# Optimization experiments

Hardware: AMD Instinct MI355X
Metric: run time of the kernel (lower is better)

The kernel has to match this reference:

```python
import jax, jax.numpy as jnp
import numpy as np
from math import sqrt


def setup_inputs() -> dict:
    key = jax.random.key(0)
    k1, k2, k3 = jax.random.split(key, 3)
    B, L, H, E = 2, 2048, 16, 64
    queries = jax.random.normal(k1, (B, L, H, E), dtype=jnp.float32)
    keys = jax.random.normal(k2, (B, L, H, E), dtype=jnp.float32)
    values = jax.random.normal(k3, (B, L, H, E), dtype=jnp.float32)
    return {"queries": queries, "keys": keys, "values": values}


def reference(queries, keys, values):
    # queries: [B,L,H,E], keys: [B,S,H,E], values: [B,S,H,D]
    B, L, H, E = queries.shape
    S = keys.shape[1]
    scale = 1.0 / sqrt(E)
    # raw scores [B,H,L,S]
    scores = jnp.einsum('blhe,bshe->bhls', queries, keys)
    # triangular causal mask (True above diagonal -> masked)
    causal = jnp.triu(jnp.ones((L, S), dtype=bool), k=1)  # [L,S]
    scores = jnp.where(causal[None, None, :, :], -jnp.inf, scores)
    A = jax.nn.softmax(scale * scores, axis=-1)  # dropout p=0 -> identity
    V = jnp.einsum('bhls,bshd->blhd', A, values)
    return V
```

## Files before the change

### kernel.cpp

```cpp
#include <hip/hip_runtime.h>

typedef __attribute__((ext_vector_type(2))) __fp16 fp16x2;
typedef __attribute__((ext_vector_type(4))) _Float16 half4;
typedef __attribute__((ext_vector_type(8))) _Float16 half8;
typedef __attribute__((ext_vector_type(4))) float floatx4;

typedef union { half8 h8; half4 h4[2]; } h8split;

#define B_SZ  2
#define L_SEQ 2048
#define NH    16
#define EDIM  64
#define LOG2E 1.4426950408889634f
#define QSCALE (0.125f * LOG2E)

__device__ __forceinline__ int swz(int s, int ch) {
    return ch ^ (((s & 7) + 2 * (s >> 4)) & 7);
}

__global__ __launch_bounds__(256, 1)
void convert_kv(const float* __restrict__ K, const float* __restrict__ V,
                _Float16* __restrict__ Kh, _Float16* __restrict__ Vt)
{
    __shared__ __align__(16) _Float16 Tile[64 * 64];
    const int st = blockIdx.x & 31;
    const int h  = (blockIdx.x >> 5) & 15;
    const int b  = blockIdx.x >> 9;
    const int s0 = st * 64;
    const int t  = threadIdx.x;
    const int r  = t >> 2, c = t & 3;
    const size_t bh   = (size_t)b * NH + h;
    const size_t src  = (((size_t)b * L_SEQ + s0 + r) * NH + h) * EDIM + c * 16;
    const size_t cbase = bh * (size_t)(L_SEQ * EDIM) + (size_t)st * 4096;

    {
        const float4* kp = (const float4*)(K + src);
        float4 f[4];
#pragma unroll
        for (int i = 0; i < 4; ++i) f[i] = kp[i];
        _Float16 tmp[16];
#pragma unroll
        for (int i = 0; i < 4; ++i) {
            fp16x2 a  = __builtin_amdgcn_cvt_pkrtz(f[i].x, f[i].y);
            fp16x2 b2 = __builtin_amdgcn_cvt_pkrtz(f[i].z, f[i].w);
            tmp[4*i+0] = (_Float16)a[0];  tmp[4*i+1] = (_Float16)a[1];
            tmp[4*i+2] = (_Float16)b2[0]; tmp[4*i+3] = (_Float16)b2[1];
        }
        _Float16* kd = Kh + cbase + (size_t)(r >> 4) * 1024 + (c >> 1) * 512 + (r & 15) * 8;
        *(half8*)(kd + (((2 * c)     & 3) * 128)) = *(half8*)&tmp[0];
        *(half8*)(kd + (((2 * c + 1) & 3) * 128)) = *(half8*)&tmp[8];
    }
    {
        const float4* vp = (const float4*)(V + src);
        float4 f[4];
#pragma unroll
        for (int i = 0; i < 4; ++i) f[i] = vp[i];
        _Float16 tmp[16];
#pragma unroll
        for (int i = 0; i < 4; ++i) {
            fp16x2 a  = __builtin_amdgcn_cvt_pkrtz(f[i].x, f[i].y);
            fp16x2 b2 = __builtin_amdgcn_cvt_pkrtz(f[i].z, f[i].w);
            tmp[4*i+0] = (_Float16)a[0];  tmp[4*i+1] = (_Float16)a[1];
            tmp[4*i+2] = (_Float16)b2[0]; tmp[4*i+3] = (_Float16)b2[1];
        }
        _Float16* base = &Tile[r * 64];
        *(half8*)(base + swz(r, 2 * c)     * 8) = *(half8*)&tmp[0];
        *(half8*)(base + swz(r, 2 * c + 1) * 8) = *(half8*)&tmp[8];
    }
    __syncthreads();
    {
        const int d = t >> 2, seg = t & 3;
        _Float16 tmp[16];
#pragma unroll
        for (int i = 0; i < 16; ++i) {
            const int s = seg * 16 + i;
            tmp[i] = Tile[s * 64 + swz(s, d >> 3) * 8 + (d & 7)];
        }
        _Float16* vd = Vt + cbase + (size_t)seg * 1024 + (d & 15) * 16 + (d >> 4) * 4;
#pragma unroll
        for (int kg = 0; kg < 4; ++kg)
            *(half4*)(vd + kg * 256) = *(half4*)&tmp[kg * 4];
    }
}

__global__ __launch_bounds__(256, 3)
void fa_fwd(const float* __restrict__ Q, const _Float16* __restrict__ Kh,
            const _Float16* __restrict__ Vt, float* __restrict__ O)
{
    __shared__ float slabL[4][4][17];
    __shared__ __align__(16) float slabO[4][16][68];

    const int i    = blockIdx.x;
    const int bh   = i & 31;
    const int tile = 31 - (i >> 5);
    const int b    = bh >> 4;
    const int h    = bh & 15;
    const int w    = threadIdx.x >> 6;
    const int lane = threadIdx.x & 63;
    const int ln16 = lane & 15;
    const int quad = lane >> 4;
    const int qrow0 = tile * 64;

    half8 qfA[4], qfB[4];
#pragma unroll
    for (int g = 0; g < 4; ++g) {
        const float4* qp = (const float4*)(Q + (((size_t)b * L_SEQ + qrow0 + g * 16 + ln16) * NH + h) * EDIM + quad * 8);
        float4 f0 = qp[0], f1 = qp[1];
        float4 f2 = qp[8], f3 = qp[9];
        fp16x2 t0 = __builtin_amdgcn_cvt_pkrtz(f0.x * QSCALE, f0.y * QSCALE);
        fp16x2 t1 = __builtin_amdgcn_cvt_pkrtz(f0.z * QSCALE, f0.w * QSCALE);
        fp16x2 t2 = __builtin_amdgcn_cvt_pkrtz(f1.x * QSCALE, f1.y * QSCALE);
        fp16x2 t3 = __builtin_amdgcn_cvt_pkrtz(f1.z * QSCALE, f1.w * QSCALE);
        qfA[g][0] = (_Float16)t0[0]; qfA[g][1] = (_Float16)t0[1];
        qfA[g][2] = (_Float16)t1[0]; qfA[g][3] = (_Float16)t1[1];
        qfA[g][4] = (_Float16)t2[0]; qfA[g][5] = (_Float16)t2[1];
        qfA[g][6] = (_Float16)t3[0]; qfA[g][7] = (_Float16)t3[1];
        t0 = __builtin_amdgcn_cvt_pkrtz(f2.x * QSCALE, f2.y * QSCALE);
        t1 = __builtin_amdgcn_cvt_pkrtz(f2.z * QSCALE, f2.w * QSCALE);
        t2 = __builtin_amdgcn_cvt_pkrtz(f3.x * QSCALE, f3.y * QSCALE);
        t3 = __builtin_amdgcn_cvt_pkrtz(f3.z * QSCALE, f3.w * QSCALE);
        qfB[g][0] = (_Float16)t0[0]; qfB[g][1] = (_Float16)t0[1];
        qfB[g][2] = (_Float16)t1[0]; qfB[g][3] = (_Float16)t1[1];
        qfB[g][4] = (_Float16)t2[0]; qfB[g][5] = (_Float16)t2[1];
        qfB[g][6] = (_Float16)t3[0]; qfB[g][7] = (_Float16)t3[1];
    }

    floatx4 acc[4][4];
#pragma unroll
    for (int dt = 0; dt < 4; ++dt)
#pragma unroll
        for (int g = 0; g < 4; ++g) acc[dt][g] = (floatx4){0.f,0.f,0.f,0.f};
    float lp[4] = {0.f, 0.f, 0.f, 0.f};

    const _Float16* kb = Kh + (size_t)bh * (L_SEQ * EDIM) + w * 1024 + lane * 8;
    const _Float16* vb = Vt + (size_t)bh * (L_SEQ * EDIM) + w * 1024 + lane * 16;
    const int nch = tile + 1;

    half8 k0c = *(const half8*)kb;
    half8 k1c = *(const half8*)(kb + 512);
    half8 v01c = *(const half8*)vb;
    half8 v23c = *(const half8*)(vb + 8);

    for (int it = 0; it < nch; ++it) {
        floatx4 st4[4];
#pragma unroll
        for (int g = 0; g < 4; ++g) {
            floatx4 z = (floatx4){0.f,0.f,0.f,0.f};
            z = __builtin_amdgcn_mfma_f32_16x16x32_f16(k0c, qfA[g], z, 0, 0, 0);
            st4[g] = __builtin_amdgcn_mfma_f32_16x16x32_f16(k1c, qfB[g], z, 0, 0, 0);
        }
        if (it + 1 < nch) {
            const _Float16* kp = kb + (size_t)(it + 1) * 4096;
            k0c = *(const half8*)kp;
            k1c = *(const half8*)(kp + 512);
        }

        const bool masked = (it == nch - 1);
        half4 pf[4];
#pragma unroll
        for (int g = 0; g < 4; ++g) {
            float p[4];
#pragma unroll
            for (int r = 0; r < 4; ++r) {
                float e = __builtin_amdgcn_exp2f(st4[g][r]);
                if (masked) {
                    const int key = it * 64 + w * 16 + quad * 4 + r;
                    e = (key <= qrow0 + g * 16 + ln16) ? e : 0.0f;
                }
                p[r] = e;
            }
            lp[g] += (p[0] + p[1]) + (p[2] + p[3]);
            fp16x2 lo = __builtin_amdgcn_cvt_pkrtz(p[0], p[1]);
            fp16x2 hi = __builtin_amdgcn_cvt_pkrtz(p[2], p[3]);
            pf[g][0] = (_Float16)lo[0]; pf[g][1] = (_Float16)lo[1];
            pf[g][2] = (_Float16)hi[0]; pf[g][3] = (_Float16)hi[1];
        }

        h8split u01, u23;
        u01.h8 = v01c;
        u23.h8 = v23c;
        const half4 vc0 = u01.h4[0];
        const half4 vc1 = u01.h4[1];
        const half4 vc2 = u23.h4[0];
        const half4 vc3 = u23.h4[1];
#pragma unroll
        for (int g = 0; g < 4; ++g)
            acc[0][g] = __builtin_amdgcn_mfma_f32_16x16x16f16(vc0, pf[g], acc[0][g], 0, 0, 0);
#pragma unroll
        for (int g = 0; g < 4; ++g)
            acc[1][g] = __builtin_amdgcn_mfma_f32_16x16x16f16(vc1, pf[g], acc[1][g], 0, 0, 0);
#pragma unroll
        for (int g = 0; g < 4; ++g)
            acc[2][g] = __builtin_amdgcn_mfma_f32_16x16x16f16(vc2, pf[g], acc[2][g], 0, 0, 0);
#pragma unroll
        for (int g = 0; g < 4; ++g)
            acc[3][g] = __builtin_amdgcn_mfma_f32_16x16x16f16(vc3, pf[g], acc[3][g], 0, 0, 0);

        if (it + 1 < nch) {
            const _Float16* vp = vb + (size_t)(it + 1) * 4096;
            v01c = *(const half8*)vp;
            v23c = *(const half8*)(vp + 8);
        }
    }

#pragma unroll
    for (int g = 0; g < 4; ++g) {
        lp[g] += __shfl_xor(lp[g], 16);
        lp[g] += __shfl_xor(lp[g], 32);
    }
    if (quad == 0) {
#pragma unroll
        for (int g = 0; g < 4; ++g) slabL[w][g][ln16] = lp[g];
    }

    const int q   = threadIdx.x >> 2;
    const int seg = threadIdx.x & 3;
    float inv = 0.f;
#pragma unroll
    for (int dt = 0; dt < 4; ++dt) {
#pragma unroll
        for (int g = 0; g < 4; ++g)
#pragma unroll
            for (int r = 0; r < 4; ++r)
                slabO[w][quad * 4 + r][g * 16 + ln16] = acc[dt][g][r];
        __syncthreads();
        if (dt == 0) {
            float lt = slabL[0][q >> 4][q & 15] + slabL[1][q >> 4][q & 15]
                     + slabL[2][q >> 4][q & 15] + slabL[3][q >> 4][q & 15];
            inv = 1.0f / lt;
        }
        float o0 = 0.f, o1 = 0.f, o2 = 0.f, o3 = 0.f;
#pragma unroll
        for (int ww = 0; ww < 4; ++ww) {
            o0 += slabO[ww][seg * 4 + 0][q];
            o1 += slabO[ww][seg * 4 + 1][q];
            o2 += slabO[ww][seg * 4 + 2][q];
            o3 += slabO[ww][seg * 4 + 3][q];
        }
        float4 ov = {o0 * inv, o1 * inv, o2 * inv, o3 * inv};
        *(float4*)(O + (((size_t)b * L_SEQ + qrow0 + q) * NH + h) * EDIM + dt * 16 + seg * 4) = ov;
        if (dt < 3) __syncthreads();
    }
}

extern "C" void kernel_launch(void* const* d_in, const int* in_sizes, int n_in,
                              void* d_out, int out_size, void* d_ws, size_t ws_size,
                              hipStream_t stream) {
    const float* Q = (const float*)d_in[0];
    const float* K = (const float*)d_in[1];
    const float* V = (const float*)d_in[2];
    float* O = (float*)d_out;
    _Float16* Kh = (_Float16*)d_ws;
    _Float16* Vt = Kh + (size_t)B_SZ * NH * L_SEQ * EDIM;
    convert_kv<<<dim3(B_SZ * NH * (L_SEQ / 64)), dim3(256), 0, stream>>>(K, V, Kh, Vt);
    fa_fwd<<<dim3(B_SZ * NH * 32), dim3(256), 0, stream>>>(Q, Kh, Vt, O);
}
```

Baseline: 124.5 us.

## Split long causal tiles across two blocks and combine partial results

Query tiles 16-31, which have the longest causal key ranges, are each split into two halves over the key chunks and run as separate blocks, in an interleaved order meant to balance load. Each half writes its unnormalized partial output and row sums to workspace, and a new combine kernel adds the halves and normalizes. This targets tail imbalance in the triangular workload and raises the block count from 1024 to 1536. The cost is an extra kernel launch and extra global traffic for the partials. There is no max-subtraction in the softmax, so the partials can simply be added.

Result: slower. 129.0 us (+3.6%).

```diff
diff --git a/kernel.cpp b/kernel.cpp
--- a/kernel.cpp
+++ b/kernel.cpp
@@ -13,6 +13,8 @@
 #define EDIM  64
 #define LOG2E 1.4426950408889634f
 #define QSCALE (0.125f * LOG2E)
+
+#define PREC 4160
 
 __device__ __forceinline__ int swz(int s, int ch) {
     return ch ^ (((s & 7) + 2 * (s >> 4)) & 7);
@@ -85,14 +87,31 @@
 
 __global__ __launch_bounds__(256, 3)
 void fa_fwd(const float* __restrict__ Q, const _Float16* __restrict__ Kh,
-            const _Float16* __restrict__ Vt, float* __restrict__ O)
+            const _Float16* __restrict__ Vt, float* __restrict__ O,
+            float* __restrict__ P)
 {
     __shared__ float slabL[4][4][17];
     __shared__ __align__(16) float slabO[4][16][68];
 
-    const int i    = blockIdx.x;
-    const int bh   = i & 31;
-    const int tile = 31 - (i >> 5);
+    const int row  = blockIdx.x >> 5;
+    const int bh   = blockIdx.x & 31;
+
+    int tile, half = 0, split = 0;
+    if (row < 4) {
+        if (row == 3) { tile = 15; }
+        else { split = 1; tile = (row == 2) ? 30 : 31; half = (row == 1); }
+    } else if (row < 39) {
+        const int g = (row - 4) / 5, pos = (row - 4) % 5, s = 15 - g;
+        if (pos == 4) { tile = s - 1; }
+        else { split = 1; tile = 2 * s - ((pos + 1) >> 1); half = (pos == 0 || pos == 2); }
+    } else if (row == 39) { split = 1; tile = 16; half = 1; }
+    else { tile = 47 - row; }
+
+    const int mid = (tile + 2) >> 1;
+    const int c0  = (split && half) ? mid : 0;
+    const int c1  = (split && !half) ? mid : tile + 1;
+    const int pidx = split ? (((bh << 4) | (tile - 16)) * 2 + half) : 0;
+
     const int b    = bh >> 4;
     const int h    = bh & 15;
     const int w    = threadIdx.x >> 6;
@@ -134,14 +153,13 @@
 
     const _Float16* kb = Kh + (size_t)bh * (L_SEQ * EDIM) + w * 1024 + lane * 8;
     const _Float16* vb = Vt + (size_t)bh * (L_SEQ * EDIM) + w * 1024 + lane * 16;
-    const int nch = tile + 1;
-
-    half8 k0c = *(const half8*)kb;
-    half8 k1c = *(const half8*)(kb + 512);
-    half8 v01c = *(const half8*)vb;
-    half8 v23c = *(const half8*)(vb + 8);
-
-    for (int it = 0; it < nch; ++it) {
+
+    half8 k0c = *(const half8*)(kb + (size_t)c0 * 4096);
+    half8 k1c = *(const half8*)(kb + (size_t)c0 * 4096 + 512);
+    half8 v01c = *(const half8*)(vb + (size_t)c0 * 4096);
+    half8 v23c = *(const half8*)(vb + (size_t)c0 * 4096 + 8);
+
+    for (int it = c0; it < c1; ++it) {
         floatx4 st4[4];
 #pragma unroll
         for (int g = 0; g < 4; ++g) {
@@ -149,13 +167,13 @@
             z = __builtin_amdgcn_mfma_f32_16x16x32_f16(k0c, qfA[g], z, 0, 0, 0);
             st4[g] = __builtin_amdgcn_mfma_f32_16x16x32_f16(k1c, qfB[g], z, 0, 0, 0);
         }
-        if (it + 1 < nch) {
+        if (it + 1 < c1) {
             const _Float16* kp = kb + (size_t)(it + 1) * 4096;
             k0c = *(const half8*)kp;
             k1c = *(const half8*)(kp + 512);
         }
 
-        const bool masked = (it == nch - 1);
+        const bool masked = (it == tile);
         half4 pf[4];
 #pragma unroll
         for (int g = 0; g < 4; ++g) {
@@ -196,7 +214,7 @@
         for (int g = 0; g < 4; ++g)
             acc[3][g] = __builtin_amdgcn_mfma_f32_16x16x16f16(vc3, pf[g], acc[3][g], 0, 0, 0);
 
-        if (it + 1 < nch) {
+        if (it + 1 < c1) {
             const _Float16* vp = vb + (size_t)(it + 1) * 4096;
             v01c = *(const half8*)vp;
             v23c = *(const half8*)(vp + 8);
@@ -227,7 +245,12 @@
         if (dt == 0) {
             float lt = slabL[0][q >> 4][q & 15] + slabL[1][q >> 4][q & 15]
                      + slabL[2][q >> 4][q & 15] + slabL[3][q >> 4][q & 15];
-            inv = 1.0f / lt;
+            if (split) {
+                if (seg == 0) P[(size_t)pidx * PREC + 4096 + q] = lt;
+                inv = 1.0f;
+            } else {
+                inv = 1.0f / lt;
+            }
         }
         float o0 = 0.f, o1 = 0.f, o2 = 0.f, o3 = 0.f;
 #pragma unroll
@@ -238,8 +261,37 @@
             o3 += slabO[ww][seg * 4 + 3][q];
         }
         float4 ov = {o0 * inv, o1 * inv, o2 * inv, o3 * inv};
-        *(float4*)(O + (((size_t)b * L_SEQ + qrow0 + q) * NH + h) * EDIM + dt * 16 + seg * 4) = ov;
+        const int d = dt * 16 + seg * 4;
+        if (split)
+            *(float4*)(P + (size_t)pidx * PREC + q * 64 + d) = ov;
+        else
+            *(float4*)(O + (((size_t)b * L_SEQ + qrow0 + q) * NH + h) * EDIM + d) = ov;
         if (dt < 3) __syncthreads();
+    }
+}
+
+__global__ __launch_bounds__(256, 1)
+void combine(const float* __restrict__ P, float* __restrict__ O)
+{
+    const int cb  = blockIdx.x;
+    const int bh  = cb & 31;
+    const int tt  = cb >> 5;
+    const int tile = 16 + tt;
+    const int b = bh >> 4, h = bh & 15;
+    const int q   = threadIdx.x >> 2;
+    const int seg = threadIdx.x & 3;
+    const float* A0 = P + (size_t)(((bh << 4) | tt) * 2) * PREC;
+    const float* A1 = A0 + PREC;
+    const float inv = 1.0f / (A0[4096 + q] + A1[4096 + q]);
+    float* op = O + (((size_t)b * L_SEQ + tile * 64 + q) * NH + h) * EDIM;
+#pragma unroll
+    for (int dt = 0; dt < 4; ++dt) {
+        const int d = dt * 16 + seg * 4;
+        float4 a = *(const float4*)(A0 + q * 64 + d);
+        float4 c = *(const float4*)(A1 + q * 64 + d);
+        float4 ov = {(a.x + c.x) * inv, (a.y + c.y) * inv,
+                     (a.z + c.z) * inv, (a.w + c.w) * inv};
+        *(float4*)(op + d) = ov;
     }
 }
 
@@ -252,6 +304,8 @@
     float* O = (float*)d_out;
     _Float16* Kh = (_Float16*)d_ws;
     _Float16* Vt = Kh + (size_t)B_SZ * NH * L_SEQ * EDIM;
+    float* P = (float*)(Vt + (size_t)B_SZ * NH * L_SEQ * EDIM);
     convert_kv<<<dim3(B_SZ * NH * (L_SEQ / 64)), dim3(256), 0, stream>>>(K, V, Kh, Vt);
-    fa_fwd<<<dim3(B_SZ * NH * 32), dim3(256), 0, stream>>>(Q, Kh, Vt, O);
-}
+    fa_fwd<<<dim3(48 * 32), dim3(256), 0, stream>>>(Q, Kh, Vt, O, P);
+    combine<<<dim3(16 * 32), dim3(256), 0, stream>>>(P, O);
+}
```

## Stage Q in LDS, interleave per-group QK/softmax/PV, raise occupancy to four blocks

Applied to the files above, without the earlier changes.

Query fragments are no longer held in registers. They are converted once into a swizzled shared-memory tile and reloaded per group inside the loop. The per-iteration loop is restructured so that each 16-row group does QK, exp and PV back to back, with the K/V prefetches spread across groups, and launch bounds rise to four blocks per CU. Tiles are also assigned in a zigzag order to balance the causal workload across consecutive blocks. The aim is lower register pressure for higher occupancy and better latency hiding, at the cost of extra LDS traffic per iteration.

After: 140.8 us. +13.1%, slower.

```diff
diff --git a/kernel.cpp b/kernel.cpp
--- a/kernel.cpp
+++ b/kernel.cpp
@@ -83,16 +83,19 @@
     }
 }
 
-__global__ __launch_bounds__(256, 3)
+__global__ __launch_bounds__(256, 4)
 void fa_fwd(const float* __restrict__ Q, const _Float16* __restrict__ Kh,
             const _Float16* __restrict__ Vt, float* __restrict__ O)
 {
     __shared__ float slabL[4][4][17];
     __shared__ __align__(16) float slabO[4][16][68];
-
-    const int i    = blockIdx.x;
-    const int bh   = i & 31;
-    const int tile = 31 - (i >> 5);
+    __shared__ __align__(16) _Float16 Qs[64 * 64];
+
+    const int i  = blockIdx.x;
+    const int bh = i & 31;
+    const int v  = i >> 5;
+    const int u  = v & 7, j = v >> 3;
+    const int tile = (j == 0) ? (31 - u) : (j == 1) ? u : (j == 2) ? (23 - u) : (8 + u);
     const int b    = bh >> 4;
     const int h    = bh & 15;
     const int w    = threadIdx.x >> 6;
@@ -100,30 +103,33 @@
     const int ln16 = lane & 15;
     const int quad = lane >> 4;
     const int qrow0 = tile * 64;
-
-    half8 qfA[4], qfB[4];
-#pragma unroll
-    for (int g = 0; g < 4; ++g) {
-        const float4* qp = (const float4*)(Q + (((size_t)b * L_SEQ + qrow0 + g * 16 + ln16) * NH + h) * EDIM + quad * 8);
-        float4 f0 = qp[0], f1 = qp[1];
-        float4 f2 = qp[8], f3 = qp[9];
-        fp16x2 t0 = __builtin_amdgcn_cvt_pkrtz(f0.x * QSCALE, f0.y * QSCALE);
-        fp16x2 t1 = __builtin_amdgcn_cvt_pkrtz(f0.z * QSCALE, f0.w * QSCALE);
-        fp16x2 t2 = __builtin_amdgcn_cvt_pkrtz(f1.x * QSCALE, f1.y * QSCALE);
-        fp16x2 t3 = __builtin_amdgcn_cvt_pkrtz(f1.z * QSCALE, f1.w * QSCALE);
-        qfA[g][0] = (_Float16)t0[0]; qfA[g][1] = (_Float16)t0[1];
-        qfA[g][2] = (_Float16)t1[0]; qfA[g][3] = (_Float16)t1[1];
-        qfA[g][4] = (_Float16)t2[0]; qfA[g][5] = (_Float16)t2[1];
-        qfA[g][6] = (_Float16)t3[0]; qfA[g][7] = (_Float16)t3[1];
-        t0 = __builtin_amdgcn_cvt_pkrtz(f2.x * QSCALE, f2.y * QSCALE);
-        t1 = __builtin_amdgcn_cvt_pkrtz(f2.z * QSCALE, f2.w * QSCALE);
-        t2 = __builtin_amdgcn_cvt_pkrtz(f3.x * QSCALE, f3.y * QSCALE);
-        t3 = __builtin_amdgcn_cvt_pkrtz(f3.z * QSCALE, f3.w * QSCALE);
-        qfB[g][0] = (_Float16)t0[0]; qfB[g][1] = (_Float16)t0[1];
-        qfB[g][2] = (_Float16)t1[0]; qfB[g][3] = (_Float16)t1[1];
-        qfB[g][4] = (_Float16)t2[0]; qfB[g][5] = (_Float16)t2[1];
-        qfB[g][6] = (_Float16)t3[0]; qfB[g][7] = (_Float16)t3[1];
-    }
+    const int nch   = tile + 1;
+
+    {
+        const int t = threadIdx.x;
+        const int r = t >> 2, c = t & 3;
+        const float4* qp = (const float4*)(Q + (((size_t)b * L_SEQ + qrow0 + r) * NH + h) * EDIM + c * 16);
+        float4 f[4];
+#pragma unroll
+        for (int k = 0; k < 4; ++k) f[k] = qp[k];
+        _Float16 tmp[16];
+#pragma unroll
+        for (int k = 0; k < 4; ++k) {
+            fp16x2 a  = __builtin_amdgcn_cvt_pkrtz(f[k].x * QSCALE, f[k].y * QSCALE);
+            fp16x2 b2 = __builtin_amdgcn_cvt_pkrtz(f[k].z * QSCALE, f[k].w * QSCALE);
+            tmp[4*k+0] = (_Float16)a[0];  tmp[4*k+1] = (_Float16)a[1];
+            tmp[4*k+2] = (_Float16)b2[0]; tmp[4*k+3] = (_Float16)b2[1];
+        }
+        const int key = (r & 7) << 3;
+        _Float16* qd = Qs + r * 64;
+        *(half8*)(qd + ((c * 16)     ^ key)) = *(half8*)&tmp[0];
+        *(half8*)(qd + ((c * 16 + 8) ^ key)) = *(half8*)&tmp[8];
+    }
+    __syncthreads();
+
+    const int qkey  = (ln16 & 7) << 3;
+    const int baseA = ln16 * 64 + ((quad * 8) ^ qkey);
+    const int baseB = ln16 * 64 + ((32 + quad * 8) ^ qkey);
 
     floatx4 acc[4][4];
 #pragma unroll
@@ -134,7 +140,6 @@
 
     const _Float16* kb = Kh + (size_t)bh * (L_SEQ * EDIM) + w * 1024 + lane * 8;
     const _Float16* vb = Vt + (size_t)bh * (L_SEQ * EDIM) + w * 1024 + lane * 16;
-    const int nch = tile + 1;
 
     half8 k0c = *(const half8*)kb;
     half8 k1c = *(const half8*)(kb + 512);
@@ -142,40 +147,9 @@
     half8 v23c = *(const half8*)(vb + 8);
 
     for (int it = 0; it < nch; ++it) {
-        floatx4 st4[4];
-#pragma unroll
-        for (int g = 0; g < 4; ++g) {
-            floatx4 z = (floatx4){0.f,0.f,0.f,0.f};
-            z = __builtin_amdgcn_mfma_f32_16x16x32_f16(k0c, qfA[g], z, 0, 0, 0);
-            st4[g] = __builtin_amdgcn_mfma_f32_16x16x32_f16(k1c, qfB[g], z, 0, 0, 0);
-        }
-        if (it + 1 < nch) {
-            const _Float16* kp = kb + (size_t)(it + 1) * 4096;
-            k0c = *(const half8*)kp;
-            k1c = *(const half8*)(kp + 512);
-        }
-
         const bool masked = (it == nch - 1);
-        half4 pf[4];
-#pragma unroll
-        for (int g = 0; g < 4; ++g) {
-            float p[4];
-#pragma unroll
-            for (int r = 0; r < 4; ++r) {
-                float e = __builtin_amdgcn_exp2f(st4[g][r]);
-                if (masked) {
-                    const int key = it * 64 + w * 16 + quad * 4 + r;
-                    e = (key <= qrow0 + g * 16 + ln16) ? e : 0.0f;
-                }
-                p[r] = e;
-            }
-            lp[g] += (p[0] + p[1]) + (p[2] + p[3]);
-            fp16x2 lo = __builtin_amdgcn_cvt_pkrtz(p[0], p[1]);
-            fp16x2 hi = __builtin_amdgcn_cvt_pkrtz(p[2], p[3]);
-            pf[g][0] = (_Float16)lo[0]; pf[g][1] = (_Float16)lo[1];
-            pf[g][2] = (_Float16)hi[0]; pf[g][3] = (_Float16)hi[1];
-        }
-
+        const half8 ka  = k0c;
+        const half8 kb2 = k1c;
         h8split u01, u23;
         u01.h8 = v01c;
         u23.h8 = v23c;
@@ -183,23 +157,47 @@
         const half4 vc1 = u01.h4[1];
         const half4 vc2 = u23.h4[0];
         const half4 vc3 = u23.h4[1];
-#pragma unroll
-        for (int g = 0; g < 4; ++g)
-            acc[0][g] = __builtin_amdgcn_mfma_f32_16x16x16f16(vc0, pf[g], acc[0][g], 0, 0, 0);
-#pragma unroll
-        for (int g = 0; g < 4; ++g)
-            acc[1][g] = __builtin_amdgcn_mfma_f32_16x16x16f16(vc1, pf[g], acc[1][g], 0, 0, 0);
-#pragma unroll
-        for (int g = 0; g < 4; ++g)
-            acc[2][g] = __builtin_amdgcn_mfma_f32_16x16x16f16(vc2, pf[g], acc[2][g], 0, 0, 0);
-#pragma unroll
-        for (int g = 0; g < 4; ++g)
-            acc[3][g] = __builtin_amdgcn_mfma_f32_16x16x16f16(vc3, pf[g], acc[3][g], 0, 0, 0);
-
-        if (it + 1 < nch) {
-            const _Float16* vp = vb + (size_t)(it + 1) * 4096;
-            v01c = *(const half8*)vp;
-            v23c = *(const half8*)(vp + 8);
+
+#pragma unroll
+        for (int g = 0; g < 4; ++g) {
+            half8 qa = *(const half8*)(Qs + baseA + g * 1024);
+            half8 qb = *(const half8*)(Qs + baseB + g * 1024);
+            floatx4 z = (floatx4){0.f,0.f,0.f,0.f};
+            z = __builtin_amdgcn_mfma_f32_16x16x32_f16(ka, qa, z, 0, 0, 0);
+            floatx4 st = __builtin_amdgcn_mfma_f32_16x16x32_f16(kb2, qb, z, 0, 0, 0);
+
+            if (g == 0 && it + 1 < nch) {
+                const _Float16* kp = kb + (size_t)(it + 1) * 4096;
+                k0c = *(const half8*)kp;
+                k1c = *(const half8*)(kp + 512);
+            }
+            if (g == 1 && it + 1 < nch) {
+                const _Float16* vp = vb + (size_t)(it + 1) * 4096;
+                v01c = *(const half8*)vp;
+                v23c = *(const half8*)(vp + 8);
+            }
+
+            float p[4];
+#pragma unroll
+            for (int r = 0; r < 4; ++r) {
+                float e = __builtin_amdgcn_exp2f(st[r]);
+                if (masked) {
+                    const int keyi = it * 64 + w * 16 + quad * 4 + r;
+                    e = (keyi <= qrow0 + g * 16 + ln16) ? e : 0.0f;
+                }
+                p[r] = e;
+            }
+            lp[g] += (p[0] + p[1]) + (p[2] + p[3]);
+            fp16x2 lo = __builtin_amdgcn_cvt_pkrtz(p[0], p[1]);
+            fp16x2 hi = __builtin_amdgcn_cvt_pkrtz(p[2], p[3]);
+            half4 pf;
+            pf[0] = (_Float16)lo[0]; pf[1] = (_Float16)lo[1];
+            pf[2] = (_Float16)hi[0]; pf[3] = (_Float16)hi[1];
+
+            acc[0][g] = __builtin_amdgcn_mfma_f32_16x16x16f16(vc0, pf, acc[0][g], 0, 0, 0);
+            acc[1][g] = __builtin_amdgcn_mfma_f32_16x16x16f16(vc1, pf, acc[1][g], 0, 0, 0);
+            acc[2][g] = __builtin_amdgcn_mfma_f32_16x16x16f16(vc2, pf, acc[2][g], 0, 0, 0);
+            acc[3][g] = __builtin_amdgcn_mfma_f32_16x16x16f16(vc3, pf, acc[3][g], 0, 0, 0);
         }
     }
 
@@ -253,5 +251,5 @@
     _Float16* Kh = (_Float16*)d_ws;
     _Float16* Vt = Kh + (size_t)B_SZ * NH * L_SEQ * EDIM;
     convert_kv<<<dim3(B_SZ * NH * (L_SEQ / 64)), dim3(256), 0, stream>>>(K, V, Kh, Vt);
-    fa_fwd<<<dim3(B_SZ * NH * 32), dim3(256), 0, stream>>>(Q, Kh, Vt, O);
-}
+    fa_fwd<<<dim3(32 * 32), dim3(256), 0, stream>>>(Q, Kh, Vt, O);
+}
```
